# Kernel tuning notes

Hardware: AMD Instinct MI355X
Metric: run time of the kernel (lower is better)

The kernel has to match this reference:

```python
import jax, jax.numpy as jnp
import numpy as np

BINS = 6
THRESH = 0.2
OUT_HW = (240, 240)


def _normalize(x, lo=0.0, hi=1.0):
    # torch: if max-min==0 return zeros, else affine rescale to [lo, hi]
    mn, mx = x.min(), x.max()
    rng = mx - mn
    safe = jnp.where(rng == 0, 1.0, rng)
    out = (x - mn) / safe * (hi - lo) + lo
    return jnp.where(rng == 0, jnp.zeros_like(x), out)


def _ponder(x):
    w = (x.max() - x.mean()) ** 2
    return _normalize(x) * w


def _zero_border(x):
    # zero first/last row and column (works batched over leading dims)
    return (x.at[..., 0, :].set(0.0)
             .at[..., :, 0].set(0.0)
             .at[..., -1, :].set(0.0)
             .at[..., :, -1].set(0.0))


def _rarity(ch):
    # ch: [H, W] single feature channel
    ch = _zero_border(ch)
    ch = _normalize(ch, 0.0, 256.0)
    # torch.histc(bins=BINS, min=0, max=256): last bin includes the max value
    bin_idx = jnp.clip(jnp.floor(ch / (256.0 / BINS)), 0, BINS - 1).astype(jnp.int32)
    hist = jnp.zeros((BINS,), ch.dtype).at[bin_idx].add(1.0)
    hist = -jnp.log(hist / hist.sum() + 0.0001)
    # (channel * bins - 1).long().clamp(0, bins-1): .long() truncates toward zero
    gidx = jnp.clip(jnp.trunc(ch * BINS - 1.0), 0, BINS - 1).astype(jnp.int32)
    dst = _normalize(hist[gidx], 0.0, 1.0)
    return _ponder(dst)


def _apply_rarity(layer):
    # layer: [1, C, H, W] -> per-channel rarity, ponderated sum, threshold
    ch = layer[0]  # [C, H, W]
    r = jax.vmap(_rarity)(ch)  # [C, H, W]
    rz = _zero_border(r)
    # channel 0 keeps its border (torch code only zeroes borders for i >= 1)
    maps = jnp.concatenate([r[:1], rz[1:]], axis=0)
    proc = jax.vmap(_ponder)(maps).sum(0)
    proc = _normalize(proc, 0.0, 1.0)
    return jnp.where(proc < THRESH, 0.0, proc)


def _group(layer):
    resized = jax.image.resize(_apply_rarity(layer), OUT_HW, 'bilinear')
    # pack of one layer: fuse_itti == map_ponderation of the single map
    return _normalize(_ponder(resized), 0.0, 256.0)


def _forward(l1, l2, l3, l4, l5):
    groups = jnp.stack([_group(l) for l in (l1, l2, l3, l4, l5)], axis=-1)  # [240,240,5]
    return groups.sum(-1), groups


def setup_inputs() -> dict:
    key = jax.random.key(0)
    ks = jax.random.split(key, 5)
    shapes = [(1, 64, 480, 480), (1, 128, 240, 240), (1, 256, 120, 120),
              (1, 512, 60, 60), (1, 512, 30, 30)]
    return {f"l{i+1}": jax.random.uniform(ks[i], shapes[i], jnp.float32)
            for i in range(5)}


def reference(l1, l2, l3, l4, l5):
    return _forward(l1, l2, l3, l4, l5)
```

## Files before the change

kernel.cpp:

```cpp
#include <hip/hip_runtime.h>
#include <math.h>

#define TPB 256

typedef float f4 __attribute__((ext_vector_type(4)));

constexpr int DIMS_[5]  = {480, 240, 120, 60, 30};
constexpr int CHS_ [5]  = {64, 128, 256, 512, 512};
constexpr int CHB_ [5]  = {0, 64, 192, 448, 960};
constexpr int TOTCH     = 1472;
constexpr int PROCB_[5] = {0, 230400, 288000, 302400, 306000};
constexpr int PROCTOT   = 306900;

constexpr int O_CHMIN = 0;
constexpr int O_CHMAX = 1472;
constexpr int O_HIST  = 2944;
constexpr int O_GCNT  = 11776;
constexpr int O_CLUT  = 20608;
constexpr int O_BSUM  = O_CLUT + 16 * 1472;
constexpr int O_PMIN  = O_BSUM + 5;
constexpr int O_PMAX  = O_PMIN + 5;
constexpr int O_S3MIN = O_PMAX + 5;
constexpr int O_S3MAX = O_S3MIN + 5;
constexpr int O_S3SUM = O_S3MAX + 5;
constexpr int O_PROC  = 44192;
constexpr int O_RESZ  = O_PROC + PROCTOT;
constexpr int N_INIT  = O_PROC + PROCTOT;

struct P {
  const float* in[5];
  float* ws;
};

#define LOAD4(d0,d1,d2,d3,p0,p1,p2,p3)                                               \
  asm volatile("global_load_dwordx4 %0, %4, off\n\t"                                 \
               "global_load_dwordx4 %1, %5, off\n\t"                                 \
               "global_load_dwordx4 %2, %6, off\n\t"                                 \
               "global_load_dwordx4 %3, %7, off"                                     \
               : "=&v"(d0), "=&v"(d1), "=&v"(d2), "=&v"(d3)                          \
               : "v"(p0), "v"(p1), "v"(p2), "v"(p3)                                  \
               : "memory")

#define WAITV4(n, a, b, c, d) do {                                                   \
    asm volatile("s_waitcnt vmcnt(" #n ")"                                           \
                 : "+v"(a), "+v"(b), "+v"(c), "+v"(d) :: "memory");                  \
    __builtin_amdgcn_sched_barrier(0);                                               \
  } while (0)

__device__ __forceinline__ void mk_hthr(float mn, float rng, float* th) {
  if (rng == 0.0f) { th[0]=th[1]=th[2]=th[3]=th[4]=INFINITY; return; }
  th[0] = mn + rng * (1.0f / 6.0f); th[1] = mn + rng * (2.0f / 6.0f);
  th[2] = mn + rng * (3.0f / 6.0f); th[3] = mn + rng * (4.0f / 6.0f);
  th[4] = mn + rng * (5.0f / 6.0f);
}
__device__ __forceinline__ void mk_gthr(float mn, float rng, float* tg) {
  if (rng == 0.0f) { tg[0]=tg[1]=tg[2]=tg[3]=tg[4]=INFINITY; return; }
  tg[0] = mn + rng * (2.0f / 1536.0f); tg[1] = mn + rng * (3.0f / 1536.0f);
  tg[2] = mn + rng * (4.0f / 1536.0f); tg[3] = mn + rng * (5.0f / 1536.0f);
  tg[4] = mn + rng * (6.0f / 1536.0f);
}

__global__ void k_init(float* ws) {
  int i = blockIdx.x * TPB + threadIdx.x;
  if (i >= N_INIT) return;
  unsigned v = 0u;
  if (i < O_CHMAX) v = 0x7F800000u;
  else if (i >= O_PMIN  && i < O_PMAX)  v = 0x7F800000u;
  else if (i >= O_S3MIN && i < O_S3MAX) v = 0x7F800000u;
  ((unsigned*)ws)[i] = v;
}

template <int L>
__device__ void bodyA(int local, const float* __restrict__ in, float* ws) {
  constexpr int D = DIMS_[L], HW = D * D, HW4 = HW / 4;
  constexpr int BPC = (HW4 + 4095) / 4096;
  constexpr int DQ = D / 4;
  int ch = local / BPC, chunk = local % BPC;
  int nvec = HW4 - chunk * 4096; if (nvec > 4096) nvec = 4096;
  int t = threadIdx.x;
  float mx = 0.0f;
  bool fullchunk = (nvec == 4096);
  if constexpr (HW4 >= 4096) {
    if (fullchunk) {
      const f4* q = (const f4*)(in + (size_t)ch * HW) + (size_t)chunk * 4096 + t;
      int base = chunk * 4096 + t;
      auto zbmx = [&](f4 v, int ii) {
        int f4i = base + ii * TPB;
        int yy = f4i / DQ, xq = f4i - yy * DQ;
        if (yy == 0 || yy == D - 1) { v.x = 0.0f; v.y = 0.0f; v.z = 0.0f; v.w = 0.0f; }
        else {
          if (xq == 0)      v.x = 0.0f;
          if (xq == DQ - 1) v.w = 0.0f;
        }
        mx = fmaxf(fmaxf(mx, fmaxf(v.x, v.y)), fmaxf(v.z, v.w));
      };
      f4 a0,a1,a2,a3, b0,b1,b2,b3, c0,c1,c2,c3, d0,d1,d2,d3;
      LOAD4(a0,a1,a2,a3, q,           q + TPB,     q + 2*TPB,  q + 3*TPB);
      LOAD4(b0,b1,b2,b3, q + 4*TPB,   q + 5*TPB,   q + 6*TPB,  q + 7*TPB);
      LOAD4(c0,c1,c2,c3, q + 8*TPB,   q + 9*TPB,   q + 10*TPB, q + 11*TPB);
      WAITV4(8, a0,a1,a2,a3);
      LOAD4(d0,d1,d2,d3, q + 12*TPB,  q + 13*TPB,  q + 14*TPB, q + 15*TPB);
      zbmx(a0,0); zbmx(a1,1); zbmx(a2,2); zbmx(a3,3);
      WAITV4(8, b0,b1,b2,b3);
      zbmx(b0,4); zbmx(b1,5); zbmx(b2,6); zbmx(b3,7);
      WAITV4(4, c0,c1,c2,c3);
      zbmx(c0,8); zbmx(c1,9); zbmx(c2,10); zbmx(c3,11);
      WAITV4(0, d0,d1,d2,d3);
      zbmx(d0,12); zbmx(d1,13); zbmx(d2,14); zbmx(d3,15);
    }
  }
  if (!fullchunk || HW4 < 4096) {
    const float4* pv = (const float4*)(in + (size_t)ch * HW) + (size_t)chunk * 4096;
    #pragma unroll 4
    for (int i = 0; i < 16; i++) {
      int vi = i * TPB + t;
      if (vi < nvec) {
        float4 v = pv[vi];
        float vv[4] = {v.x, v.y, v.z, v.w};
        int f4i = chunk * 4096 + vi;
        if constexpr (D % 4 == 0) {
          int y = f4i / DQ, xq = f4i - y * DQ;
          if (y == 0 || y == D - 1) { vv[0] = vv[1] = vv[2] = vv[3] = 0.0f; }
          else {
            if (xq == 0)      vv[0] = 0.0f;
            if (xq == DQ - 1) vv[3] = 0.0f;
          }
        } else {
          int e0 = f4i * 4;
          #pragma unroll
          for (int j = 0; j < 4; j++) {
            int e = e0 + j, y = e / D, x = e - y * D;
            bool inr = ((unsigned)(x - 1) < (unsigned)(D - 2)) && ((unsigned)(y - 1) < (unsigned)(D - 2));
            if (!inr) vv[j] = 0.0f;
          }
        }
        #pragma unroll
        for (int j = 0; j < 4; j++) mx = fmaxf(mx, vv[j]);
      }
    }
  }
  for (int o = 32; o; o >>= 1) mx = fmaxf(mx, __shfl_down(mx, o));
  __shared__ float smx[4];
  int w = t >> 6;
  if ((t & 63) == 0) smx[w] = mx;
  __syncthreads();
  if (t == 0) {
    mx = fmaxf(fmaxf(smx[0], smx[1]), fmaxf(smx[2], smx[3]));
    atomicMax((unsigned*)ws + O_CHMAX + CHB_[L] + ch, __float_as_uint(mx));
  }
}
__global__ __launch_bounds__(TPB, 4) void kA(P p) {
  int b = blockIdx.x;
  if      (b <  960) bodyA<0>(b,        p.in[0], p.ws);
  else if (b < 1472) bodyA<1>(b -  960, p.in[1], p.ws);
  else if (b < 1728) bodyA<2>(b - 1472, p.in[2], p.ws);
  else if (b < 2240) bodyA<3>(b - 1728, p.in[3], p.ws);
  else               bodyA<4>(b - 2240, p.in[4], p.ws);
}

template <int L>
__device__ void bodyB(int local, const float* __restrict__ in, float* ws) {
  constexpr int D = DIMS_[L], HW = D * D, HW4 = HW / 4;
  constexpr int BPC = (HW4 + 4095) / 4096;
  constexpr int DQ = D / 4;
  int ch = local / BPC, chunk = local % BPC;
  int g = CHB_[L] + ch;
  float rng = ws[O_CHMAX + g];
  float th[5], tg[5];
  mk_hthr(0.0f, rng, th);
  mk_gthr(0.0f, rng, tg);
  int nvec = HW4 - chunk * 4096; if (nvec > 4096) nvec = 4096;
  int t = threadIdx.x;
  unsigned c[10] = {0u,0u,0u,0u,0u,0u,0u,0u,0u,0u};
  unsigned nval = 0u;
  auto cnt1 = [&](float x) {
    #pragma unroll
    for (int k = 0; k < 5; k++) { c[k] += (x >= th[k]); c[5 + k] += (x >= tg[k]); }
  };
  bool fullchunk = (nvec == 4096);
  if constexpr (HW4 >= 4096) {
    if (fullchunk) {
      const f4* q = (const f4*)(in + (size_t)ch * HW) + (size_t)chunk * 4096 + t;
      int base = chunk * 4096 + t;
      auto zbcnt = [&](f4 v, int ii) {
        int f4i = base + ii * TPB;
        int yy = f4i / DQ, xq = f4i - yy * DQ;
        if (yy == 0 || yy == D - 1) { v.x = 0.0f; v.y = 0.0f; v.z = 0.0f; v.w = 0.0f; }
        else {
          if (xq == 0)      v.x = 0.0f;
          if (xq == DQ - 1) v.w = 0.0f;
        }
        cnt1(v.x); cnt1(v.y); cnt1(v.z); cnt1(v.w);
      };
      f4 a0,a1,a2,a3, b0,b1,b2,b3, c0,c1,c2,c3, d0,d1,d2,d3;
      LOAD4(a0,a1,a2,a3, q,           q + TPB,     q + 2*TPB,  q + 3*TPB);
      LOAD4(b0,b1,b2,b3, q + 4*TPB,   q + 5*TPB,   q + 6*TPB,  q + 7*TPB);
      LOAD4(c0,c1,c2,c3, q + 8*TPB,   q + 9*TPB,   q + 10*TPB, q + 11*TPB);
      WAITV4(8, a0,a1,a2,a3);
      LOAD4(d0,d1,d2,d3, q + 12*TPB,  q + 13*TPB,  q + 14*TPB, q + 15*TPB);
      zbcnt(a0,0); zbcnt(a1,1); zbcnt(a2,2); zbcnt(a3,3);
      WAITV4(8, b0,b1,b2,b3);
      zbcnt(b0,4); zbcnt(b1,5); zbcnt(b2,6); zbcnt(b3,7);
      WAITV4(4, c0,c1,c2,c3);
      zbcnt(c0,8); zbcnt(c1,9); zbcnt(c2,10); zbcnt(c3,11);
      WAITV4(0, d0,d1,d2,d3);
      zbcnt(d0,12); zbcnt(d1,13); zbcnt(d2,14); zbcnt(d3,15);
      nval = 64u;
    }
  }
  if (!fullchunk || HW4 < 4096) {
    const float4* pv = (const float4*)(in + (size_t)ch * HW) + (size_t)chunk * 4096;
    #pragma unroll 4
    for (int i = 0; i < 16; i++) {
      int vi = i * TPB + t;
      if (vi < nvec) {
        float4 v = pv[vi];
        float vv[4] = {v.x, v.y, v.z, v.w};
        int f4i = chunk * 4096 + vi;
        if constexpr (D % 4 == 0) {
          int y = f4i / DQ, xq = f4i - y * DQ;
          if (y == 0 || y == D - 1) { vv[0] = vv[1] = vv[2] = vv[3] = 0.0f; }
          else {
            if (xq == 0)      vv[0] = 0.0f;
            if (xq == DQ - 1) vv[3] = 0.0f;
          }
        } else {
          int e0 = f4i * 4;
          #pragma unroll
          for (int j = 0; j < 4; j++) {
            int e = e0 + j, y = e / D, x = e - y * D;
            bool inr = ((unsigned)(x - 1) < (unsigned)(D - 2)) && ((unsigned)(y - 1) < (unsigned)(D - 2));
            if (!inr) vv[j] = 0.0f;
          }
        }
        nval += 4u;
        cnt1(vv[0]); cnt1(vv[1]); cnt1(vv[2]); cnt1(vv[3]);
      }
    }
  }
  #pragma unroll
  for (int k = 0; k < 10; k++)
    for (int o = 32; o; o >>= 1) c[k] += __shfl_down(c[k], o);
  for (int o = 32; o; o >>= 1) nval += __shfl_down(nval, o);
  if ((t & 63) == 0) {
    unsigned* H = (unsigned*)ws + O_HIST + g * 6;
    unsigned* G = (unsigned*)ws + O_GCNT + g * 6;
    atomicAdd(H + 0, nval - c[0]); atomicAdd(H + 1, c[0] - c[1]);
    atomicAdd(H + 2, c[1] - c[2]); atomicAdd(H + 3, c[2] - c[3]);
    atomicAdd(H + 4, c[3] - c[4]); atomicAdd(H + 5, c[4]);
    atomicAdd(G + 0, nval - c[5]); atomicAdd(G + 1, c[5] - c[6]);
    atomicAdd(G + 2, c[6] - c[7]); atomicAdd(G + 3, c[7] - c[8]);
    atomicAdd(G + 4, c[8] - c[9]); atomicAdd(G + 5, c[9]);
  }
}
__global__ __launch_bounds__(TPB, 4) void kB(P p) {
  int b = blockIdx.x;
  if      (b <  960) bodyB<0>(b,        p.in[0], p.ws);
  else if (b < 1472) bodyB<1>(b -  960, p.in[1], p.ws);
  else if (b < 1728) bodyB<2>(b - 1472, p.in[2], p.ws);
  else if (b < 2240) bodyB<3>(b - 1728, p.in[3], p.ws);
  else               bodyB<4>(b - 2240, p.in[4], p.ws);
}

__global__ void kS(P p) {
  int ch = blockIdx.x * TPB + threadIdx.x;
  if (ch >= TOTCH) return;
  float* ws = p.ws;
  int l = (ch < 64) ? 0 : (ch < 192) ? 1 : (ch < 448) ? 2 : (ch < 960) ? 3 : 4;
  int D = DIMS_[l];
  int HW = D * D;
  int c0 = ch - CHB_[l];
  unsigned hc[6], gc[6];
  unsigned* H = (unsigned*)ws + O_HIST + ch * 6;
  unsigned* G = (unsigned*)ws + O_GCNT + ch * 6;
  #pragma unroll
  for (int k = 0; k < 6; k++) { hc[k] = H[k]; gc[k] = G[k]; }
  float HWf = (float)HW;
  float nh[6];
  #pragma unroll
  for (int k = 0; k < 6; k++) nh[k] = -logf((float)hc[k] / HWf + 1e-4f);
  float dmn = INFINITY, dmx = -INFINITY;
  #pragma unroll
  for (int k = 0; k < 6; k++) if (gc[k]) { dmn = fminf(dmn, nh[k]); dmx = fmaxf(dmx, nh[k]); }
  float dr = dmx - dmn;
  float dstn[6];
  #pragma unroll
  for (int k = 0; k < 6; k++) dstn[k] = (dr == 0.0f) ? 0.0f : ((nh[k] - dmn) / dr);
  float maxv = (dr == 0.0f) ? 0.0f : 1.0f;
  double s1 = 0.0;
  #pragma unroll
  for (int k = 0; k < 6; k++) s1 += (double)gc[k] * (double)dstn[k];
  float mean1 = (float)(s1 / (double)HW);
  float w1 = maxv - mean1; w1 *= w1;
  float lut1[6];
  #pragma unroll
  for (int k = 0; k < 6; k++) lut1[k] = dstn[k] * w1;
  float mxc = ws[O_CHMAX + ch];
  float tg[5];
  mk_gthr(0.0f, mxc, tg);
  int gb = (0.0f >= tg[0]) + (0.0f >= tg[1]) + (0.0f >= tg[2]) + (0.0f >= tg[3]) + (0.0f >= tg[4]);
  unsigned bcnt = (unsigned)(4 * D - 4);
  float lmn, lmx;
  double s2 = 0.0;
  if (c0 == 0) {
    lmn = INFINITY; lmx = -INFINITY;
    #pragma unroll
    for (int k = 0; k < 6; k++) if (gc[k]) {
      lmn = fminf(lmn, lut1[k]); lmx = fmaxf(lmx, lut1[k]);
      s2 += (double)gc[k] * (double)lut1[k];
    }
  } else {
    lmn = 0.0f; lmx = 0.0f;
    #pragma unroll
    for (int k = 0; k < 6; k++) {
      unsigned ic = gc[k] - ((k == gb) ? bcnt : 0u);
      if (ic) {
        lmn = fminf(lmn, lut1[k]); lmx = fmaxf(lmx, lut1[k]);
        s2 += (double)ic * (double)lut1[k];
      }
    }
  }
  float mean2 = (float)(s2 / (double)HW);
  float w2 = lmx - mean2; w2 *= w2;
  float r2 = lmx - lmn;
  float lout[6];
  #pragma unroll
  for (int k = 0; k < 6; k++) lout[k] = (r2 == 0.0f) ? 0.0f : (((lut1[k] - lmn) / r2) * w2);
  float* T = ws + O_CLUT + (size_t)ch * 16;
  #pragma unroll
  for (int k = 0; k < 5; k++) T[5 + k] = tg[k];
  #pragma unroll
  for (int k = 0; k < 6; k++) T[10 + k] = lout[k];
  float bc = (c0 == 0) ? lout[gb] : ((r2 == 0.0f) ? 0.0f : (((0.0f - lmn) / r2) * w2));
  atomicAdd(ws + O_BSUM + l, bc);
}

template <int L>
__device__ void bodyC(int local, const float* __restrict__ in, float* ws,
                      float* slut, float* sred) {
  constexpr int D = DIMS_[L], HW = D * D, HW4 = HW / 4, C = CHS_[L];
  constexpr int NT  = (HW4 + 63) / 64;
  constexpr int NCH = C / 64;
  int tile = local % NT, chunk = local / NT;
  int cbase = CHB_[L] + chunk * 64;
  int t = threadIdx.x, lane = t & 63, w = t >> 6;
  const float* gl = ws + O_CLUT + (size_t)cbase * 16;
  for (int i = t; i < 1024; i += TPB) slut[i] = gl[i];
  __syncthreads();
  int p4 = tile * 64 + lane;
  bool valid = p4 < HW4;
  float a0 = 0.0f, a1 = 0.0f, a2 = 0.0f, a3 = 0.0f;
  if (valid) {
    const float4* bp = (const float4*)in + (size_t)(chunk * 64 + w * 16) * HW4 + p4;
    const float* su = slut + (w * 16) * 16;
    #pragma unroll 4
    for (int c = 0; c < 16; c++) {
      float4 v = bp[(size_t)c * HW4];
      const float* cl = su + c * 16 + 5;
      float g0 = cl[0], g1 = cl[1], g2 = cl[2], g3 = cl[3], g4 = cl[4];
      float l0 = cl[5], l1 = cl[6], l2 = cl[7], l3 = cl[8], l4 = cl[9], l5 = cl[10];
      float s;
      s = (v.x >= g0) ? l1 : l0; s = (v.x >= g1) ? l2 : s; s = (v.x >= g2) ? l3 : s;
      s = (v.x >= g3) ? l4 : s;  s = (v.x >= g4) ? l5 : s; a0 += s;
      s = (v.y >= g0) ? l1 : l0; s = (v.y >= g1) ? l2 : s; s = (v.y >= g2) ? l3 : s;
      s = (v.y >= g3) ? l4 : s;  s = (v.y >= g4) ? l5 : s; a1 += s;
      s = (v.z >= g0) ? l1 : l0; s = (v.z >= g1) ? l2 : s; s = (v.z >= g2) ? l3 : s;
      s = (v.z >= g3) ? l4 : s;  s = (v.z >= g4) ? l5 : s; a2 += s;
      s = (v.w >= g0) ? l1 : l0; s = (v.w >= g1) ? l2 : s; s = (v.w >= g2) ? l3 : s;
      s = (v.w >= g3) ? l4 : s;  s = (v.w >= g4) ? l5 : s; a3 += s;
    }
  }
  sred[0 * 256 + w * 64 + lane] = a0;
  sred[1 * 256 + w * 64 + lane] = a1;
  sred[2 * 256 + w * 64 + lane] = a2;
  sred[3 * 256 + w * 64 + lane] = a3;
  __syncthreads();
  if (w == 0 && valid) {
    float o[4];
    #pragma unroll
    for (int j = 0; j < 4; j++)
      o[j] = sred[j * 256 + lane] + sred[j * 256 + 64 + lane] +
             sred[j * 256 + 128 + lane] + sred[j * 256 + 192 + lane];
    float bs = ws[O_BSUM + L];
    float* procL = ws + O_PROC + PROCB_[L];
    int px0 = p4 * 4;
    if constexpr (NCH == 1) {
      #pragma unroll
      for (int j = 0; j < 4; j++) {
        int px = px0 + j, y = px / D, x = px - y * D;
        bool inr = ((unsigned)(x - 1) < (unsigned)(D - 2)) && ((unsigned)(y - 1) < (unsigned)(D - 2));
        if (!inr) o[j] = bs;
      }
      ((float4*)procL)[p4] = make_float4(o[0], o[1], o[2], o[3]);
    } else {
      #pragma unroll
      for (int j = 0; j < 4; j++) {
        int px = px0 + j, y = px / D, x = px - y * D;
        bool inr = ((unsigned)(x - 1) < (unsigned)(D - 2)) && ((unsigned)(y - 1) < (unsigned)(D - 2));
        if (inr) atomicAdd(procL + px, o[j]);
        else if (chunk == 0) procL[px] = bs;
      }
    }
  }
}
__global__ __launch_bounds__(TPB) void kC(P p) {
  __shared__ float slut[1024];
  __shared__ float sred[1024];
  int b = blockIdx.x;
  if      (b <  900) bodyC<0>(b,        p.in[0], p.ws, slut, sred);
  else if (b < 1350) bodyC<1>(b -  900, p.in[1], p.ws, slut, sred);
  else if (b < 1578) bodyC<2>(b - 1350, p.in[2], p.ws, slut, sred);
  else if (b < 1698) bodyC<3>(b - 1578, p.in[3], p.ws, slut, sred);
  else               bodyC<4>(b - 1698, p.in[4], p.ws, slut, sred);
}

template <int L>
__device__ void bodyD(int chunk, float* ws) {
  constexpr int HW = DIMS_[L] * DIMS_[L];
  const float* pr = ws + O_PROC + PROCB_[L];
  int t = threadIdx.x;
  float mn = INFINITY, mx = 0.0f;
  #pragma unroll
  for (int i = 0; i < 16; i++) {
    int idx = chunk * 4096 + i * TPB + t;
    if (idx < HW) { float v = pr[idx]; mn = fminf(mn, v); mx = fmaxf(mx, v); }
  }
  for (int o = 32; o; o >>= 1) { mn = fminf(mn, __shfl_down(mn, o)); mx = fmaxf(mx, __shfl_down(mx, o)); }
  __shared__ float smn[4], smx[4];
  int w = t >> 6;
  if ((t & 63) == 0) { smn[w] = mn; smx[w] = mx; }
  __syncthreads();
  if (t == 0) {
    mn = fminf(fminf(smn[0], smn[1]), fminf(smn[2], smn[3]));
    mx = fmaxf(fmaxf(smx[0], smx[1]), fmaxf(smx[2], smx[3]));
    atomicMin((unsigned*)ws + O_PMIN + L, __float_as_uint(mn));
    atomicMax((unsigned*)ws + O_PMAX + L, __float_as_uint(mx));
  }
}
__global__ void kD(P p) {
  int b = blockIdx.x;
  if      (b < 57) bodyD<0>(b,      p.ws);
  else if (b < 72) bodyD<1>(b - 57, p.ws);
  else if (b < 76) bodyD<2>(b - 72, p.ws);
  else if (b < 77) bodyD<3>(b - 76, p.ws);
  else             bodyD<4>(b - 77, p.ws);
}

template <int L>
__device__ float bodyF(int px, float* ws) {
  constexpr int D = DIMS_[L];
  constexpr float INV = (float)D / 240.0f;
  constexpr float KS = (INV > 1.0f) ? INV : 1.0f;
  int oy = px / 240, ox = px - oy * 240;
  float mnv = __uint_as_float(((unsigned*)ws)[O_PMIN + L]);
  float mxv = __uint_as_float(((unsigned*)ws)[O_PMAX + L]);
  float pr = mxv - mnv;
  const float* procL = ws + O_PROC + PROCB_[L];
  float sfy = ((float)oy + 0.5f) * INV - 0.5f;
  float sfx = ((float)ox + 0.5f) * INV - 0.5f;
  int y0 = (int)ceilf(sfy - KS);  if (y0 < 0) y0 = 0;
  int y1 = (int)floorf(sfy + KS); if (y1 > D - 1) y1 = D - 1;
  int x0 = (int)ceilf(sfx - KS);  if (x0 < 0) x0 = 0;
  int x1 = (int)floorf(sfx + KS); if (x1 > D - 1) x1 = D - 1;
  float wsx = 0.0f;
  for (int jx = x0; jx <= x1; jx++) wsx += fmaxf(1.0f - fabsf(sfx - (float)jx) / KS, 0.0f);
  float acc = 0.0f, wsy = 0.0f;
  for (int jy = y0; jy <= y1; jy++) {
    float wy = fmaxf(1.0f - fabsf(sfy - (float)jy) / KS, 0.0f);
    wsy += wy;
    if (wy > 0.0f) {
      const float* row = procL + jy * D;
      float rs = 0.0f;
      for (int jx = x0; jx <= x1; jx++) {
        float wx = fmaxf(1.0f - fabsf(sfx - (float)jx) / KS, 0.0f);
        if (wx > 0.0f) {
          float v = row[jx];
          float tv = (pr == 0.0f) ? 0.0f : ((v - mnv) / pr);
          tv = (tv < 0.2f) ? 0.0f : tv;
          rs += wx * tv;
        }
      }
      acc += wy * rs;
    }
  }
  return acc / (wsy * wsx);
}
__global__ void kF(P p) {
  float* ws = p.ws;
  int b = blockIdx.x, l = b / 225;
  int px = (b - l * 225) * TPB + threadIdx.x;
  float res;
  switch (l) {
    case 0: res = bodyF<0>(px, ws); break;
    case 1: res = bodyF<1>(px, ws); break;
    case 2: res = bodyF<2>(px, ws); break;
    case 3: res = bodyF<3>(px, ws); break;
    default: res = bodyF<4>(px, ws); break;
  }
  ws[O_RESZ + l * 57600 + px] = res;
  float mn = res, mx = res, s = res;
  for (int o = 32; o; o >>= 1) {
    mn = fminf(mn, __shfl_down(mn, o));
    mx = fmaxf(mx, __shfl_down(mx, o));
    s += __shfl_down(s, o);
  }
  __shared__ float smn[4], smx[4], ssm[4];
  int t = threadIdx.x, w = t >> 6;
  if ((t & 63) == 0) { smn[w] = mn; smx[w] = mx; ssm[w] = s; }
  __syncthreads();
  if (t == 0) {
    mn = fminf(fminf(smn[0], smn[1]), fminf(smn[2], smn[3]));
    mx = fmaxf(fmaxf(smx[0], smx[1]), fmaxf(smx[2], smx[3]));
    s = ssm[0] + ssm[1] + ssm[2] + ssm[3];
    atomicMin((unsigned*)ws + O_S3MIN + l, __float_as_uint(mn));
    atomicMax((unsigned*)ws + O_S3MAX + l, __float_as_uint(mx));
    atomicAdd(ws + O_S3SUM + l, s);
  }
}

__global__ void kG2(P p, float* __restrict__ out) {
  float* ws = p.ws;
  int px = blockIdx.x * TPB + threadIdx.x;
  float sum = 0.0f;
  #pragma unroll
  for (int l = 0; l < 5; l++) {
    float v = ws[O_RESZ + l * 57600 + px];
    float mn3 = __uint_as_float(((unsigned*)ws)[O_S3MIN + l]);
    float mx3 = __uint_as_float(((unsigned*)ws)[O_S3MAX + l]);
    float mean3 = ws[O_S3SUM + l] / 57600.0f;
    float r3 = mx3 - mn3;
    float ov;
    if (r3 == 0.0f) ov = 0.0f;
    else {
      float w3 = mx3 - mean3; w3 *= w3;
      if (w3 == 0.0f) ov = 0.0f;
      else ov = ((v - mn3) / r3) * w3 / w3 * 256.0f;
    }
    out[57600 + px * 5 + l] = ov;
    sum += ov;
  }
  out[px] = sum;
}

extern "C" void kernel_launch(void* const* d_in, const int* in_sizes, int n_in,
                              void* d_out, int out_size, void* d_ws, size_t ws_size,
                              hipStream_t stream) {
  (void)in_sizes; (void)n_in; (void)out_size; (void)ws_size;
  P p;
  for (int i = 0; i < 5; i++) p.in[i] = (const float*)d_in[i];
  p.ws = (float*)d_ws;
  float* out = (float*)d_out;

  k_init<<<(N_INIT + TPB - 1) / TPB, TPB, 0, stream>>>(p.ws);
  kA  <<<2752, TPB, 0, stream>>>(p);
  kB  <<<2752, TPB, 0, stream>>>(p);
  kS  <<<6,    TPB, 0, stream>>>(p);
  kC  <<<1730, TPB, 0, stream>>>(p);
  kD  <<<78,   TPB, 0, stream>>>(p);
  kF  <<<1125, TPB, 0, stream>>>(p);
  kG2 <<<225,  TPB, 0, stream>>>(p, out);
}
```

Measured before the change: 289.7 us.

## Cache packed per-pixel bin indices in histogram pass to shrink LUT-pass reads

```diff
diff --git a/kernel.cpp b/kernel.cpp
--- a/kernel.cpp
+++ b/kernel.cpp
@@ -11,6 +11,9 @@
 constexpr int TOTCH     = 1472;
 constexpr int PROCB_[5] = {0, 230400, 288000, 302400, 306000};
 constexpr int PROCTOT   = 306900;
+
+constexpr int GF4B_[5] = {0, 3686400, 5529600, 6451200, 6912000};
+constexpr int TOTF4    = 7027200;
 
 constexpr int O_CHMIN = 0;
 constexpr int O_CHMAX = 1472;
@@ -26,6 +29,8 @@
 constexpr int O_PROC  = 44192;
 constexpr int O_RESZ  = O_PROC + PROCTOT;
 constexpr int N_INIT  = O_PROC + PROCTOT;
+constexpr int O_GIDX  = O_RESZ + 5 * 57600;
+constexpr size_t NEED_WS_BYTES = (size_t)(O_GIDX + TOTF4) * 4;
 
 struct P {
   const float* in[5];
@@ -158,7 +163,7 @@
   else               bodyA<4>(b - 2240, p.in[4], p.ws);
 }
 
-template <int L>
+template <int L, bool GX>
 __device__ void bodyB(int local, const float* __restrict__ in, float* ws) {
   constexpr int D = DIMS_[L], HW = D * D, HW4 = HW / 4;
   constexpr int BPC = (HW4 + 4095) / 4096;
@@ -173,16 +178,24 @@
   int t = threadIdx.x;
   unsigned c[10] = {0u,0u,0u,0u,0u,0u,0u,0u,0u,0u};
   unsigned nval = 0u;
-  auto cnt1 = [&](float x) {
+  auto cnt1g = [&](float x) -> unsigned {
+    unsigned gx = 0u;
     #pragma unroll
-    for (int k = 0; k < 5; k++) { c[k] += (x >= th[k]); c[5 + k] += (x >= tg[k]); }
+    for (int k = 0; k < 5; k++) {
+      c[k] += (x >= th[k]);
+      unsigned b = (x >= tg[k]);
+      c[5 + k] += b;
+      gx += b;
+    }
+    return gx;
   };
+  unsigned* gp = (unsigned*)(ws + O_GIDX) + GF4B_[L] + (size_t)ch * HW4 + (size_t)chunk * 4096;
   bool fullchunk = (nvec == 4096);
   if constexpr (HW4 >= 4096) {
     if (fullchunk) {
       const f4* q = (const f4*)(in + (size_t)ch * HW) + (size_t)chunk * 4096 + t;
       int base = chunk * 4096 + t;
-      auto zbcnt = [&](f4 v, int ii) {
+      auto zbcntg = [&](f4 v, int ii) -> unsigned {
         int f4i = base + ii * TPB;
         int yy = f4i / DQ, xq = f4i - yy * DQ;
         if (yy == 0 || yy == D - 1) { v.x = 0.0f; v.y = 0.0f; v.z = 0.0f; v.w = 0.0f; }
@@ -190,21 +203,30 @@
           if (xq == 0)      v.x = 0.0f;
           if (xq == DQ - 1) v.w = 0.0f;
         }
-        cnt1(v.x); cnt1(v.y); cnt1(v.z); cnt1(v.w);
+        unsigned g0 = cnt1g(v.x), g1 = cnt1g(v.y), g2 = cnt1g(v.z), g3 = cnt1g(v.w);
+        return g0 | (g1 << 8) | (g2 << 16) | (g3 << 24);
       };
       f4 a0,a1,a2,a3, b0,b1,b2,b3, c0,c1,c2,c3, d0,d1,d2,d3;
+      unsigned pk0,pk1,pk2,pk3, pk4,pk5,pk6,pk7, pk8,pk9,pk10,pk11, pk12,pk13,pk14,pk15;
       LOAD4(a0,a1,a2,a3, q,           q + TPB,     q + 2*TPB,  q + 3*TPB);
       LOAD4(b0,b1,b2,b3, q + 4*TPB,   q + 5*TPB,   q + 6*TPB,  q + 7*TPB);
       LOAD4(c0,c1,c2,c3, q + 8*TPB,   q + 9*TPB,   q + 10*TPB, q + 11*TPB);
       WAITV4(8, a0,a1,a2,a3);
       LOAD4(d0,d1,d2,d3, q + 12*TPB,  q + 13*TPB,  q + 14*TPB, q + 15*TPB);
-      zbcnt(a0,0); zbcnt(a1,1); zbcnt(a2,2); zbcnt(a3,3);
+      pk0 = zbcntg(a0,0); pk1 = zbcntg(a1,1); pk2 = zbcntg(a2,2); pk3 = zbcntg(a3,3);
       WAITV4(8, b0,b1,b2,b3);
-      zbcnt(b0,4); zbcnt(b1,5); zbcnt(b2,6); zbcnt(b3,7);
+      pk4 = zbcntg(b0,4); pk5 = zbcntg(b1,5); pk6 = zbcntg(b2,6); pk7 = zbcntg(b3,7);
       WAITV4(4, c0,c1,c2,c3);
-      zbcnt(c0,8); zbcnt(c1,9); zbcnt(c2,10); zbcnt(c3,11);
+      pk8 = zbcntg(c0,8); pk9 = zbcntg(c1,9); pk10 = zbcntg(c2,10); pk11 = zbcntg(c3,11);
       WAITV4(0, d0,d1,d2,d3);
-      zbcnt(d0,12); zbcnt(d1,13); zbcnt(d2,14); zbcnt(d3,15);
+      pk12 = zbcntg(d0,12); pk13 = zbcntg(d1,13); pk14 = zbcntg(d2,14); pk15 = zbcntg(d3,15);
+      if constexpr (GX) {
+        unsigned* gq = gp + t;
+        gq[0]       = pk0;  gq[TPB]     = pk1;  gq[2*TPB]  = pk2;  gq[3*TPB]  = pk3;
+        gq[4*TPB]   = pk4;  gq[5*TPB]   = pk5;  gq[6*TPB]  = pk6;  gq[7*TPB]  = pk7;
+        gq[8*TPB]   = pk8;  gq[9*TPB]   = pk9;  gq[10*TPB] = pk10; gq[11*TPB] = pk11;
+        gq[12*TPB]  = pk12; gq[13*TPB]  = pk13; gq[14*TPB] = pk14; gq[15*TPB] = pk15;
+      }
       nval = 64u;
     }
   }
@@ -234,7 +256,8 @@
           }
         }
         nval += 4u;
-        cnt1(vv[0]); cnt1(vv[1]); cnt1(vv[2]); cnt1(vv[3]);
+        unsigned g0 = cnt1g(vv[0]), g1 = cnt1g(vv[1]), g2 = cnt1g(vv[2]), g3 = cnt1g(vv[3]);
+        if constexpr (GX) gp[vi] = g0 | (g1 << 8) | (g2 << 16) | (g3 << 24);
       }
     }
   }
@@ -253,13 +276,14 @@
     atomicAdd(G + 4, c[8] - c[9]); atomicAdd(G + 5, c[9]);
   }
 }
+template <bool GX>
 __global__ __launch_bounds__(TPB, 4) void kB(P p) {
   int b = blockIdx.x;
-  if      (b <  960) bodyB<0>(b,        p.in[0], p.ws);
-  else if (b < 1472) bodyB<1>(b -  960, p.in[1], p.ws);
-  else if (b < 1728) bodyB<2>(b - 1472, p.in[2], p.ws);
-  else if (b < 2240) bodyB<3>(b - 1728, p.in[3], p.ws);
-  else               bodyB<4>(b - 2240, p.in[4], p.ws);
+  if      (b <  960) bodyB<0, GX>(b,        p.in[0], p.ws);
+  else if (b < 1472) bodyB<1, GX>(b -  960, p.in[1], p.ws);
+  else if (b < 1728) bodyB<2, GX>(b - 1472, p.in[2], p.ws);
+  else if (b < 2240) bodyB<3, GX>(b - 1728, p.in[3], p.ws);
+  else               bodyB<4, GX>(b - 2240, p.in[4], p.ws);
 }
 
 __global__ void kS(P p) {
@@ -335,7 +359,7 @@
   atomicAdd(ws + O_BSUM + l, bc);
 }
 
-template <int L>
+template <int L, bool GX>
 __device__ void bodyC(int local, const float* __restrict__ in, float* ws,
                       float* slut, float* sred) {
   constexpr int D = DIMS_[L], HW = D * D, HW4 = HW / 4, C = CHS_[L];
@@ -351,23 +375,37 @@
   bool valid = p4 < HW4;
   float a0 = 0.0f, a1 = 0.0f, a2 = 0.0f, a3 = 0.0f;
   if (valid) {
-    const float4* bp = (const float4*)in + (size_t)(chunk * 64 + w * 16) * HW4 + p4;
     const float* su = slut + (w * 16) * 16;
-    #pragma unroll 4
-    for (int c = 0; c < 16; c++) {
-      float4 v = bp[(size_t)c * HW4];
-      const float* cl = su + c * 16 + 5;
-      float g0 = cl[0], g1 = cl[1], g2 = cl[2], g3 = cl[3], g4 = cl[4];
-      float l0 = cl[5], l1 = cl[6], l2 = cl[7], l3 = cl[8], l4 = cl[9], l5 = cl[10];
-      float s;
-      s = (v.x >= g0) ? l1 : l0; s = (v.x >= g1) ? l2 : s; s = (v.x >= g2) ? l3 : s;
-      s = (v.x >= g3) ? l4 : s;  s = (v.x >= g4) ? l5 : s; a0 += s;
-      s = (v.y >= g0) ? l1 : l0; s = (v.y >= g1) ? l2 : s; s = (v.y >= g2) ? l3 : s;
-      s = (v.y >= g3) ? l4 : s;  s = (v.y >= g4) ? l5 : s; a1 += s;
-      s = (v.z >= g0) ? l1 : l0; s = (v.z >= g1) ? l2 : s; s = (v.z >= g2) ? l3 : s;
-      s = (v.z >= g3) ? l4 : s;  s = (v.z >= g4) ? l5 : s; a2 += s;
-      s = (v.w >= g0) ? l1 : l0; s = (v.w >= g1) ? l2 : s; s = (v.w >= g2) ? l3 : s;
-      s = (v.w >= g3) ? l4 : s;  s = (v.w >= g4) ? l5 : s; a3 += s;
+    if constexpr (GX) {
+      const unsigned* gp = (const unsigned*)(ws + O_GIDX) + GF4B_[L] +
+                           (size_t)(chunk * 64 + w * 16) * HW4 + p4;
+      #pragma unroll 4
+      for (int c = 0; c < 16; c++) {
+        unsigned pk = gp[(size_t)c * HW4];
+        const float* cl = su + c * 16 + 10;
+        a0 += cl[pk & 7u];
+        a1 += cl[(pk >> 8) & 7u];
+        a2 += cl[(pk >> 16) & 7u];
+        a3 += cl[(pk >> 24) & 7u];
+      }
+    } else {
+      const float4* bp = (const float4*)in + (size_t)(chunk * 64 + w * 16) * HW4 + p4;
+      #pragma unroll 4
+      for (int c = 0; c < 16; c++) {
+        float4 v = bp[(size_t)c * HW4];
+        const float* cl = su + c * 16 + 5;
+        float g0 = cl[0], g1 = cl[1], g2 = cl[2], g3 = cl[3], g4 = cl[4];
+        float l0 = cl[5], l1 = cl[6], l2 = cl[7], l3 = cl[8], l4 = cl[9], l5 = cl[10];
+        float s;
+        s = (v.x >= g0) ? l1 : l0; s = (v.x >= g1) ? l2 : s; s = (v.x >= g2) ? l3 : s;
+        s = (v.x >= g3) ? l4 : s;  s = (v.x >= g4) ? l5 : s; a0 += s;
+        s = (v.y >= g0) ? l1 : l0; s = (v.y >= g1) ? l2 : s; s = (v.y >= g2) ? l3 : s;
+        s = (v.y >= g3) ? l4 : s;  s = (v.y >= g4) ? l5 : s; a1 += s;
+        s = (v.z >= g0) ? l1 : l0; s = (v.z >= g1) ? l2 : s; s = (v.z >= g2) ? l3 : s;
+        s = (v.z >= g3) ? l4 : s;  s = (v.z >= g4) ? l5 : s; a2 += s;
+        s = (v.w >= g0) ? l1 : l0; s = (v.w >= g1) ? l2 : s; s = (v.w >= g2) ? l3 : s;
+        s = (v.w >= g3) ? l4 : s;  s = (v.w >= g4) ? l5 : s; a3 += s;
+      }
     }
   }
   sred[0 * 256 + w * 64 + lane] = a0;
@@ -403,15 +441,16 @@
     }
   }
 }
+template <bool GX>
 __global__ __launch_bounds__(TPB) void kC(P p) {
   __shared__ float slut[1024];
   __shared__ float sred[1024];
   int b = blockIdx.x;
-  if      (b <  900) bodyC<0>(b,        p.in[0], p.ws, slut, sred);
-  else if (b < 1350) bodyC<1>(b -  900, p.in[1], p.ws, slut, sred);
-  else if (b < 1578) bodyC<2>(b - 1350, p.in[2], p.ws, slut, sred);
-  else if (b < 1698) bodyC<3>(b - 1578, p.in[3], p.ws, slut, sred);
-  else               bodyC<4>(b - 1698, p.in[4], p.ws, slut, sred);
+  if      (b <  900) bodyC<0, GX>(b,        p.in[0], p.ws, slut, sred);
+  else if (b < 1350) bodyC<1, GX>(b -  900, p.in[1], p.ws, slut, sred);
+  else if (b < 1578) bodyC<2, GX>(b - 1350, p.in[2], p.ws, slut, sred);
+  else if (b < 1698) bodyC<3, GX>(b - 1578, p.in[3], p.ws, slut, sred);
+  else               bodyC<4, GX>(b - 1698, p.in[4], p.ws, slut, sred);
 }
 
 template <int L>
@@ -545,17 +584,24 @@
 extern "C" void kernel_launch(void* const* d_in, const int* in_sizes, int n_in,
                               void* d_out, int out_size, void* d_ws, size_t ws_size,
                               hipStream_t stream) {
-  (void)in_sizes; (void)n_in; (void)out_size; (void)ws_size;
+  (void)in_sizes; (void)n_in; (void)out_size;
   P p;
   for (int i = 0; i < 5; i++) p.in[i] = (const float*)d_in[i];
   p.ws = (float*)d_ws;
   float* out = (float*)d_out;
+  bool gx = ws_size >= NEED_WS_BYTES;
 
   k_init<<<(N_INIT + TPB - 1) / TPB, TPB, 0, stream>>>(p.ws);
   kA  <<<2752, TPB, 0, stream>>>(p);
-  kB  <<<2752, TPB, 0, stream>>>(p);
-  kS  <<<6,    TPB, 0, stream>>>(p);
-  kC  <<<1730, TPB, 0, stream>>>(p);
+  if (gx) {
+    kB<true> <<<2752, TPB, 0, stream>>>(p);
+    kS       <<<6,    TPB, 0, stream>>>(p);
+    kC<true> <<<1730, TPB, 0, stream>>>(p);
+  } else {
+    kB<false><<<2752, TPB, 0, stream>>>(p);
+    kS       <<<6,    TPB, 0, stream>>>(p);
+    kC<false><<<1730, TPB, 0, stream>>>(p);
+  }
   kD  <<<78,   TPB, 0, stream>>>(p);
   kF  <<<1125, TPB, 0, stream>>>(p);
   kG2 <<<225,  TPB, 0, stream>>>(p, out);
```

Result: slower. 308.4 us (+6.4%).
